# Performance work log

Hardware: AMD Instinct MI355X
Metric: run time of the kernel (lower is better)

The kernel has to match this reference:

```python
import jax, jax.numpy as jnp
import numpy as np

EPS = 1e-12  # torch F.normalize eps

def _l2norm(t):
    # normalize along last axis, clamp norm like torch.nn.functional.normalize
    n = jnp.sqrt(jnp.sum(t * t, axis=-1, keepdims=True))
    return t / jnp.maximum(n, EPS)

def setup_inputs() -> dict:
    key = jax.random.key(0)
    k1, k2, k3 = jax.random.split(key, 3)
    B, N, C, h = 4, 16384, 512, 8
    x = jax.random.normal(k1, (B, N, C), dtype=jnp.float32)
    qkv_w = jax.random.normal(k2, (C, 3 * C), dtype=jnp.float32) * 0.02
    proj_w = jax.random.normal(k3, (C, C), dtype=jnp.float32) * 0.02
    proj_b = jnp.zeros((C,), dtype=jnp.float32)
    temperature = jnp.ones((h, 1, 1), dtype=jnp.float32)  # temperature_init=1.0
    return {"x": x, "H": 128, "W": 128, "qkv_w": qkv_w,
            "proj_w": proj_w, "proj_b": proj_b, "temperature": temperature}

def reference(x, H, W, qkv_w, proj_w, proj_b, temperature):
    B, N, C = x.shape
    h = temperature.shape[0]
    d = C // h
    qkv = (x @ qkv_w).reshape(B, N, 3, h, d)          # [B,N,3,h,d]
    qkv = jnp.transpose(qkv, (2, 0, 3, 1, 4))         # [3,B,h,N,d]
    q, k, v = qkv[0], qkv[1], qkv[2]
    # channel attention: transpose to [B,h,d,N], normalize over tokens
    q = _l2norm(jnp.swapaxes(q, -2, -1))              # [B,h,d,N]
    k = _l2norm(jnp.swapaxes(k, -2, -1))              # [B,h,d,N]
    v = jnp.swapaxes(v, -2, -1)                       # [B,h,d,N]
    attn = jnp.einsum('bhdn,bhen->bhde', q, k) * temperature  # [B,h,d,d]
    attn = jax.nn.softmax(attn, axis=-1)
    out = jnp.einsum('bhde,bhen->bhdn', attn, v)      # [B,h,d,N]
    out = jnp.transpose(out, (0, 3, 1, 2)).reshape(B, N, C)
    return out @ proj_w + proj_b
```

## Files before the change

kernel.cpp:

```cpp
#include <hip/hip_runtime.h>
#include <stdint.h>
#include <stddef.h>


typedef unsigned short u16;
typedef __attribute__((ext_vector_type(8))) unsigned short u16x8;
typedef __attribute__((ext_vector_type(8))) __bf16 bf16x8;
typedef __attribute__((ext_vector_type(4))) float f32x4;

#define B_DIM 4
#define N_TOK 16384
#define C_DIM 512
#define CQ3   1536
#define NROWS 65536

__device__ __forceinline__ u16 f2bf(float f) {
  union { float f; uint32_t u; } v; v.f = f;
  uint32_t r = v.u + 0x7FFFu + ((v.u >> 16) & 1u);
  return (u16)(r >> 16);
}
__device__ __forceinline__ float bf2f(u16 u) {
  union { uint32_t u; float f; } v; v.u = ((uint32_t)u) << 16;
  return v.f;
}
__device__ __forceinline__ bf16x8 as_bf16x8(u16x8 u) {
  union { u16x8 u; bf16x8 b; } v; v.u = u; return v.b;
}
__device__ __forceinline__ bf16x8 ldfrag(const u16* p) {
  return as_bf16x8(*(const u16x8*)p);
}
__device__ __forceinline__ void gl_lds16(const void* g, void* l) {
  __builtin_amdgcn_global_load_lds(
      (const __attribute__((address_space(1))) uint32_t*)g,
      (__attribute__((address_space(3))) uint32_t*)l, 16, 0, 0);
}

__global__ __launch_bounds__(256) void k_wswz(const float* __restrict__ w, u16* __restrict__ wl) {
  int g = blockIdx.x * 256 + threadIdx.x;
  int c8 = g / CQ3, j = g - c8 * CQ3;
  u16x8 o;
#pragma unroll
  for (int i = 0; i < 8; ++i) o[i] = f2bf(w[(size_t)(c8 * 8 + i) * CQ3 + j]);
  *(u16x8*)(wl + (size_t)g * 8) = o;
}
__global__ __launch_bounds__(256) void k_pswz(const float* __restrict__ w, u16* __restrict__ pwl) {
  int g = blockIdx.x * 256 + threadIdx.x;
  int d8 = g >> 9, j = g & 511;
  u16x8 o;
#pragma unroll
  for (int i = 0; i < 8; ++i) o[i] = f2bf(w[(size_t)(d8 * 8 + i) * 512 + j]);
  *(u16x8*)(pwl + (size_t)g * 8) = o;
}
__global__ __launch_bounds__(256) void k_vswz(const float* __restrict__ w, u16* __restrict__ vA) {
  int g = blockIdx.x * 256 + threadIdx.x;
  int c = g >> 6, q = g & 63;
  const float* s = w + (size_t)c * CQ3 + 1024 + q * 8;
  float4 v0 = *(const float4*)s, v1 = *(const float4*)(s + 4);
  u16x8 o;
  o[0] = f2bf(v0.x); o[1] = f2bf(v0.y); o[2] = f2bf(v0.z); o[3] = f2bf(v0.w);
  o[4] = f2bf(v1.x); o[5] = f2bf(v1.y); o[6] = f2bf(v1.z); o[7] = f2bf(v1.w);
  *(u16x8*)(vA + (size_t)g * 8) = o;
}

__global__ __launch_bounds__(256) void k_xc(const float* __restrict__ x,
                                            u16* __restrict__ xb,
                                            u16* __restrict__ xbT) {
  __shared__ __align__(16) u16 T[16384];
  const int bi = blockIdx.x;
  const int b = bi >> 9, tt = (bi >> 2) & 127, ct = bi & 3;
  const int n0 = tt * 128, c0 = ct * 128;
  const int tid = threadIdx.x;
  const int cb8 = (tid & 15) * 8;
  const int tch = tid >> 4;
  const float* src = x + (size_t)(b * N_TOK + n0 + tch * 8) * C_DIM + c0 + cb8;
  float v[8][8];
#pragma unroll
  for (int j = 0; j < 8; ++j) {
    float4 a0 = *(const float4*)(src + (size_t)j * C_DIM);
    float4 a1 = *(const float4*)(src + (size_t)j * C_DIM + 4);
    v[j][0] = a0.x; v[j][1] = a0.y; v[j][2] = a0.z; v[j][3] = a0.w;
    v[j][4] = a1.x; v[j][5] = a1.y; v[j][6] = a1.z; v[j][7] = a1.w;
  }
  u16* xbd = xb + (size_t)(b * N_TOK + n0 + tch * 8) * C_DIM + c0 + cb8;
#pragma unroll
  for (int j = 0; j < 8; ++j) {
    u16x8 o;
#pragma unroll
    for (int i = 0; i < 8; ++i) o[i] = f2bf(v[j][i]);
    *(u16x8*)(xbd + (size_t)j * C_DIM) = o;
  }
#pragma unroll
  for (int i = 0; i < 8; ++i) {
    int c_loc = cb8 + i;
    int pc = tch ^ (tid & 15);
    u16x8 o;
#pragma unroll
    for (int j = 0; j < 8; ++j) o[j] = f2bf(v[j][i]);
    *(u16x8*)&T[c_loc * 128 + pc * 8] = o;
  }
  __syncthreads();
#pragma unroll
  for (int t = 0; t < 8; ++t) {
    int c_loc = t * 16 + (tid >> 4);
    int lch = tid & 15;
    int pc = lch ^ ((c_loc >> 3) & 15);
    u16x8 o = *(const u16x8*)&T[c_loc * 128 + pc * 8];
    *(u16x8*)&xbT[(size_t)(b * C_DIM + c0 + c_loc) * N_TOK + n0 + lch * 8] = o;
  }
}

__global__ __launch_bounds__(256, 4) void k_g(const u16* __restrict__ xbT, u16* __restrict__ Gp) {
  __shared__ __align__(16) u16 As[8192];
  __shared__ __align__(16) u16 Bs[8192];
  const int tid = threadIdx.x, lane = tid & 63, wid = tid >> 6;
  const int orig = blockIdx.x;
  const int wg = (orig & 7) * 128 + (orig >> 3);
  const int kc = wg >> 6, rem = wg & 63;
  const int b = rem >> 4, ti = (rem >> 2) & 3, tj = rem & 3;
  const u16* abase = xbT + ((size_t)b * 512 + ti * 128) * N_TOK + kc * 1024;
  const u16* bbase = xbT + ((size_t)b * 512 + tj * 128) * N_TOK + kc * 1024;
  const int wr = wid >> 1, wc = wid & 1;

  f32x4 acc[4][4];
#pragma unroll
  for (int i = 0; i < 4; ++i)
#pragma unroll
    for (int j = 0; j < 4; ++j) acc[i][j] = (f32x4){0.f, 0.f, 0.f, 0.f};

  for (int kb = 0; kb < 16; ++kb) {
#pragma unroll
    for (int s4 = 0; s4 < 4; ++s4) {
      int slot = s4 * 256 + tid;
      int idx = slot >> 3, kblk = slot & 7;
      int kcol = kb * 64 + ((kblk ^ (idx & 7)) * 8);
      gl_lds16(abase + (size_t)idx * N_TOK + kcol, &As[slot * 8]);
      gl_lds16(bbase + (size_t)idx * N_TOK + kcol, &Bs[slot * 8]);
    }
    __syncthreads();
#pragma unroll
    for (int kk = 0; kk < 2; ++kk) {
      const int krow = kk * 4 + (lane >> 4);
      const int pk = krow ^ (lane & 7);
      bf16x8 af[4], bfr[4];
#pragma unroll
      for (int t = 0; t < 4; ++t)
        af[t] = *(const bf16x8*)&As[((wr * 64 + t * 16 + (lane & 15)) * 8 + pk) * 8];
#pragma unroll
      for (int t = 0; t < 4; ++t)
        bfr[t] = *(const bf16x8*)&Bs[((wc * 64 + t * 16 + (lane & 15)) * 8 + pk) * 8];
#pragma unroll
      for (int mt = 0; mt < 4; ++mt)
#pragma unroll
        for (int nt = 0; nt < 4; ++nt)
          acc[mt][nt] = __builtin_amdgcn_mfma_f32_16x16x32_bf16(af[mt], bfr[nt], acc[mt][nt], 0, 0, 0);
    }
    __syncthreads();
  }
  u16* wsl = (wid < 2) ? &As[wid * 4096] : &Bs[(wid - 2) * 4096];
#pragma unroll
  for (int mt = 0; mt < 4; ++mt)
#pragma unroll
    for (int nt = 0; nt < 4; ++nt)
#pragma unroll
      for (int r = 0; r < 4; ++r) {
        int row = mt * 16 + (lane >> 4) * 4 + r;
        int col = nt * 16 + (lane & 15);
        int slot = (col >> 3) ^ (row & 7);
        wsl[row * 64 + slot * 8 + (col & 7)] = f2bf(acc[mt][nt][r]);
      }
  u16* gdst = Gp + (size_t)(kc * 4 + b) * 262144;
#pragma unroll
  for (int it = 0; it < 8; ++it) {
    int rr = it * 8 + (lane >> 3);
    int slot = (lane & 7) ^ (rr & 7);
    *(u16x8*)&gdst[(size_t)(ti * 128 + wr * 64 + rr) * 512 + tj * 128 + wc * 64 + (lane & 7) * 8] =
        *(const u16x8*)&wsl[rr * 64 + slot * 8];
  }
}

__global__ __launch_bounds__(256) void k_red(const u16* __restrict__ Gp, u16* __restrict__ G) {
  int g = blockIdx.x * 256 + threadIdx.x;
  int b = g >> 15;
  size_t off = (size_t)(g & 32767) * 8;
  float s[8];
#pragma unroll
  for (int i = 0; i < 8; ++i) s[i] = 0.f;
  for (int kc = 0; kc < 16; ++kc) {
    u16x8 v = *(const u16x8*)(Gp + (size_t)(kc * 4 + b) * 262144 + off);
#pragma unroll
    for (int i = 0; i < 8; ++i) s[i] += bf2f(v[i]);
  }
  u16x8 o;
#pragma unroll
  for (int i = 0; i < 8; ++i) o[i] = f2bf(s[i]);
  *(u16x8*)(G + (size_t)b * 262144 + off) = o;
}

__global__ __launch_bounds__(256) void k_gq(const u16* __restrict__ G,
                                            const u16* __restrict__ wl,
                                            u16* __restrict__ Gqk) {
  const int bi = blockIdx.x;
  const int b = bi >> 5, mt = (bi >> 3) & 3, nt2 = bi & 7;
  const int m0 = mt * 128, n0 = nt2 * 128;
  const int lane = threadIdx.x & 63, w = threadIdx.x >> 6;
  f32x4 acc[8][2];
#pragma unroll
  for (int i = 0; i < 8; ++i) { acc[i][0] = (f32x4){0,0,0,0}; acc[i][1] = (f32x4){0,0,0,0}; }
  for (int ks = 0; ks < 16; ++ks) {
    bf16x8 bfr[2];
#pragma unroll
    for (int nf = 0; nf < 2; ++nf)
      bfr[nf] = ldfrag(wl + ((size_t)(ks * 4 + (lane >> 4)) * CQ3 + n0 + w * 32 + nf * 16 + (lane & 15)) * 8);
#pragma unroll
    for (int mf = 0; mf < 8; ++mf) {
      bf16x8 af = ldfrag(G + (size_t)b * 262144 + (size_t)(m0 + mf * 16 + (lane & 15)) * 512 + ks * 32 + (lane >> 4) * 8);
#pragma unroll
      for (int nf = 0; nf < 2; ++nf)
        acc[mf][nf] = __builtin_amdgcn_mfma_f32_16x16x32_bf16(af, bfr[nf], acc[mf][nf], 0, 0, 0);
    }
  }
#pragma unroll
  for (int mf = 0; mf < 8; ++mf)
#pragma unroll
    for (int nf = 0; nf < 2; ++nf)
#pragma unroll
      for (int r = 0; r < 4; ++r) {
        int d = m0 + mf * 16 + (lane >> 4) * 4 + r;
        int j = n0 + w * 32 + nf * 16 + (lane & 15);
        Gqk[(size_t)b * 524288 + ((size_t)(d >> 3) * 1024 + j) * 8 + (d & 7)] = f2bf(acc[mf][nf][r]);
      }
}

__global__ __launch_bounds__(256) void k_s2(const u16* __restrict__ Gqk,
                                            const u16* __restrict__ wl,
                                            const u16* __restrict__ pwl,
                                            const float* __restrict__ temp,
                                            u16* __restrict__ Ml) {
  __shared__ float Ssh[4][4096];
  __shared__ u16 At[64 * 72];
  __shared__ float ssqsh[128];
  __shared__ float rqk[128];
  const int tid = threadIdx.x, lane = tid & 63, w = tid >> 6;
  const int bh = blockIdx.x, b = bh >> 3, hh = bh & 7;
  if (tid < 128) ssqsh[tid] = 0.f;

  f32x4 acc[4][4];
#pragma unroll
  for (int i = 0; i < 4; ++i)
#pragma unroll
    for (int j = 0; j < 4; ++j) acc[i][j] = (f32x4){0.f, 0.f, 0.f, 0.f};
  for (int ks = 0; ks < 4; ++ks) {
    const int crow = w * 16 + ks * 4 + (lane >> 4);
    bf16x8 aq[4], bk[4];
#pragma unroll
    for (int mf = 0; mf < 4; ++mf)
      aq[mf] = ldfrag(wl + ((size_t)crow * CQ3 + hh * 64 + mf * 16 + (lane & 15)) * 8);
#pragma unroll
    for (int nf = 0; nf < 4; ++nf)
      bk[nf] = ldfrag(Gqk + (size_t)b * 524288 + ((size_t)crow * 1024 + 512 + hh * 64 + nf * 16 + (lane & 15)) * 8);
#pragma unroll
    for (int mf = 0; mf < 4; ++mf)
#pragma unroll
      for (int nf = 0; nf < 4; ++nf)
        acc[mf][nf] = __builtin_amdgcn_mfma_f32_16x16x32_bf16(aq[mf], bk[nf], acc[mf][nf], 0, 0, 0);
  }
#pragma unroll
  for (int mf = 0; mf < 4; ++mf)
#pragma unroll
    for (int nf = 0; nf < 4; ++nf)
#pragma unroll
      for (int r = 0; r < 4; ++r)
        Ssh[w][(mf * 16 + (lane >> 4) * 4 + r) * 64 + nf * 16 + (lane & 15)] = acc[mf][nf][r];
  __syncthreads();
  for (int idx = tid; idx < 4096; idx += 256)
    Ssh[0][idx] = Ssh[0][idx] + Ssh[1][idx] + Ssh[2][idx] + Ssh[3][idx];

  {
    const int d = tid & 63, part = tid >> 6;
    float sq = 0.f, sk = 0.f;
    for (int co = 0; co < 16; ++co) {
      int c8 = part * 16 + co;
      u16x8 wq = *(const u16x8*)(wl + ((size_t)c8 * CQ3 + hh * 64 + d) * 8);
      u16x8 gq = *(const u16x8*)(Gqk + (size_t)b * 524288 + ((size_t)c8 * 1024 + hh * 64 + d) * 8);
      u16x8 wk = *(const u16x8*)(wl + ((size_t)c8 * CQ3 + 512 + hh * 64 + d) * 8);
      u16x8 gk = *(const u16x8*)(Gqk + (size_t)b * 524288 + ((size_t)c8 * 1024 + 512 + hh * 64 + d) * 8);
#pragma unroll
      for (int i = 0; i < 8; ++i) {
        sq += bf2f(wq[i]) * bf2f(gq[i]);
        sk += bf2f(wk[i]) * bf2f(gk[i]);
      }
    }
    atomicAdd(&ssqsh[d], sq);
    atomicAdd(&ssqsh[64 + d], sk);
  }
  __syncthreads();
  if (tid < 128) rqk[tid] = 1.f / fmaxf(sqrtf(fmaxf(ssqsh[tid], 0.f)), 1e-12f);
  __syncthreads();

  {
    const float tp = temp[hh];
    const int d = tid >> 2, q4 = tid & 3;
    float vals[16];
    float mx = -3.0e38f;
    const float rqd = rqk[d];
#pragma unroll
    for (int i = 0; i < 16; ++i) {
      float v = Ssh[0][d * 64 + q4 * 16 + i] * rqd * rqk[64 + q4 * 16 + i] * tp;
      vals[i] = v; mx = fmaxf(mx, v);
    }
    mx = fmaxf(mx, __shfl_xor(mx, 1));
    mx = fmaxf(mx, __shfl_xor(mx, 2));
    float sum = 0.f;
#pragma unroll
    for (int i = 0; i < 16; ++i) { vals[i] = __expf(vals[i] - mx); sum += vals[i]; }
    sum += __shfl_xor(sum, 1);
    sum += __shfl_xor(sum, 2);
    const float inv = 1.f / sum;
#pragma unroll
    for (int i = 0; i < 16; ++i) At[(q4 * 16 + i) * 72 + d] = f2bf(vals[i] * inv);
  }
  __syncthreads();

  f32x4 acc2[4][8];
#pragma unroll
  for (int i = 0; i < 4; ++i)
#pragma unroll
    for (int j = 0; j < 8; ++j) acc2[i][j] = (f32x4){0.f, 0.f, 0.f, 0.f};
#pragma unroll
  for (int s = 0; s < 2; ++s) {
    bf16x8 af[4], bfr[8];
#pragma unroll
    for (int mf = 0; mf < 4; ++mf)
      af[mf] = *(const bf16x8*)&At[(mf * 16 + (lane & 15)) * 72 + s * 32 + (lane >> 4) * 8];
#pragma unroll
    for (int nf = 0; nf < 8; ++nf)
      bfr[nf] = ldfrag(pwl + ((size_t)(hh * 8 + s * 4 + (lane >> 4)) * 512 + w * 128 + nf * 16 + (lane & 15)) * 8);
#pragma unroll
    for (int mf = 0; mf < 4; ++mf)
#pragma unroll
      for (int nf = 0; nf < 8; ++nf)
        acc2[mf][nf] = __builtin_amdgcn_mfma_f32_16x16x32_bf16(af[mf], bfr[nf], acc2[mf][nf], 0, 0, 0);
  }
#pragma unroll
  for (int mf = 0; mf < 4; ++mf)
#pragma unroll
    for (int nf = 0; nf < 8; ++nf)
#pragma unroll
      for (int r = 0; r < 4; ++r) {
        int e = mf * 16 + (lane >> 4) * 4 + r;
        int j = w * 128 + nf * 16 + (lane & 15);
        int cc = hh * 64 + e;
        Ml[(size_t)b * 262144 + ((size_t)(cc >> 3) * 512 + j) * 8 + (cc & 7)] = f2bf(acc2[mf][nf][r]);
      }
}

__global__ __launch_bounds__(256) void k_p(const u16* __restrict__ vA,
                                           const u16* __restrict__ Ml,
                                           u16* __restrict__ Pl) {
  const int bi = blockIdx.x;
  const int b = bi >> 4, ct = (bi >> 2) & 3, jt = bi & 3;
  const int m0 = ct * 128, j0 = jt * 128;
  const int lane = threadIdx.x & 63, w = threadIdx.x >> 6;
  f32x4 acc[8][2];
#pragma unroll
  for (int i = 0; i < 8; ++i) { acc[i][0] = (f32x4){0,0,0,0}; acc[i][1] = (f32x4){0,0,0,0}; }
  for (int ks = 0; ks < 16; ++ks) {
    bf16x8 bfr[2];
#pragma unroll
    for (int nf = 0; nf < 2; ++nf)
      bfr[nf] = ldfrag(Ml + (size_t)b * 262144 + ((size_t)(ks * 4 + (lane >> 4)) * 512 + j0 + w * 32 + nf * 16 + (lane & 15)) * 8);
#pragma unroll
    for (int mf = 0; mf < 8; ++mf) {
      bf16x8 af = ldfrag(vA + (size_t)(m0 + mf * 16 + (lane & 15)) * 512 + ks * 32 + (lane >> 4) * 8);
#pragma unroll
      for (int nf = 0; nf < 2; ++nf)
        acc[mf][nf] = __builtin_amdgcn_mfma_f32_16x16x32_bf16(af, bfr[nf], acc[mf][nf], 0, 0, 0);
    }
  }
#pragma unroll
  for (int mf = 0; mf < 8; ++mf)
#pragma unroll
    for (int nf = 0; nf < 2; ++nf)
#pragma unroll
      for (int r = 0; r < 4; ++r) {
        int c = m0 + mf * 16 + (lane >> 4) * 4 + r;
        int j = j0 + w * 32 + nf * 16 + (lane & 15);
        Pl[(size_t)b * 262144 + ((size_t)(c >> 3) * 512 + j) * 8 + (c & 7)] = f2bf(acc[mf][nf][r]);
      }
}

__global__ __launch_bounds__(256, 4) void k_out(const u16* __restrict__ xb,
                                                const u16* __restrict__ Pl,
                                                const float* __restrict__ pb,
                                                float* __restrict__ out) {
  __shared__ __align__(16) u16 As[8192];
  __shared__ __align__(16) u16 Bs[8192];
  const int tid = threadIdx.x;
  const int orig = blockIdx.x;
  const int wg = (orig & 7) * 256 + (orig >> 3);
  const int cb = wg & 3, rb = wg >> 2;
  const int row0 = rb * 128, col0 = cb * 128;
  const int b = rb >> 7;
  const int lane = tid & 63, wid = tid >> 6;
  const int wr = wid >> 1, wc = wid & 1;
  float bias[4];
#pragma unroll
  for (int nt = 0; nt < 4; ++nt) bias[nt] = pb[col0 + wc * 64 + nt * 16 + (lane & 15)];

  f32x4 acc[4][4];
#pragma unroll
  for (int i = 0; i < 4; ++i)
#pragma unroll
    for (int j = 0; j < 4; ++j) acc[i][j] = (f32x4){0.f, 0.f, 0.f, 0.f};

  const u16* pbase = Pl + (size_t)b * 262144;
  for (int kb = 0; kb < 8; ++kb) {
#pragma unroll
    for (int s4 = 0; s4 < 4; ++s4) {
      int slot = s4 * 256 + tid;
      int idx = slot >> 3, kblk = slot & 7;
      gl_lds16(xb + (size_t)(row0 + idx) * C_DIM + kb * 64 + ((kblk ^ (idx & 7)) * 8), &As[slot * 8]);
      int kblkB = slot >> 7, j = slot & 127;
      gl_lds16(pbase + ((size_t)(kb * 8 + kblkB) * 512 + col0 + j) * 8, &Bs[slot * 8]);
    }
    __syncthreads();
#pragma unroll
    for (int kk = 0; kk < 2; ++kk) {
      const int krow = kk * 4 + (lane >> 4);
      const int pk = krow ^ (lane & 7);
      bf16x8 af[4], bfr[4];
#pragma unroll
      for (int t = 0; t < 4; ++t)
        af[t] = *(const bf16x8*)&As[((wr * 64 + t * 16 + (lane & 15)) * 8 + pk) * 8];
#pragma unroll
      for (int t = 0; t < 4; ++t)
        bfr[t] = *(const bf16x8*)&Bs[(krow * 128 + wc * 64 + t * 16 + (lane & 15)) * 8];
#pragma unroll
      for (int mt = 0; mt < 4; ++mt)
#pragma unroll
        for (int nt = 0; nt < 4; ++nt)
          acc[mt][nt] = __builtin_amdgcn_mfma_f32_16x16x32_bf16(af[mt], bfr[nt], acc[mt][nt], 0, 0, 0);
    }
    __syncthreads();
  }
  float* slice = (wid < 2) ? (float*)&As[wid * 4096] : (float*)&Bs[(wid - 2) * 4096];
#pragma unroll
  for (int half = 0; half < 2; ++half) {
#pragma unroll
    for (int m2 = 0; m2 < 2; ++m2)
#pragma unroll
      for (int nt = 0; nt < 4; ++nt)
#pragma unroll
        for (int r = 0; r < 4; ++r) {
          int row = m2 * 16 + (lane >> 4) * 4 + r;
          int col = nt * 16 + (lane & 15);
          int slot = (col >> 2) ^ (row & 15);
          slice[row * 64 + slot * 4 + (col & 3)] = acc[half * 2 + m2][nt][r] + bias[nt];
        }
#pragma unroll
    for (int it = 0; it < 8; ++it) {
      int rr = it * 4 + (lane >> 4);
      int s = (lane & 15) ^ (rr & 15);
      *(float4*)&out[(size_t)(row0 + wr * 64 + half * 32 + rr) * C_DIM + col0 + wc * 64 + (lane & 15) * 4] =
          *(const float4*)&slice[rr * 64 + s * 4];
    }
  }
}

extern "C" void kernel_launch(void* const* d_in, const int* in_sizes, int n_in,
                              void* d_out, int out_size, void* d_ws, size_t ws_size,
                              hipStream_t stream) {
  const float* x      = (const float*)d_in[0];
  const float* qkv_w  = (const float*)d_in[3];
  const float* proj_w = (const float*)d_in[4];
  const float* proj_b = (const float*)d_in[5];
  const float* temp   = (const float*)d_in[6];
  float* out = (float*)d_out;

  char* ws = (char*)d_ws;
  u16* xb  = (u16*)(ws);
  u16* xbT = (u16*)(ws + 67108864);
  u16* wl  = (u16*)(ws + 134217728);
  u16* pwl = (u16*)(ws + 135790592);
  u16* vA  = (u16*)(ws + 136314880);
  u16* Gp  = (u16*)(ws + 136839168);
  u16* G   = (u16*)(ws + 170393600);
  u16* Gqk = (u16*)(ws + 172490752);
  u16* Ml  = (u16*)(ws + 176685056);
  u16* Pl  = (u16*)(ws + 178782208);

  k_wswz<<<384, 256, 0, stream>>>(qkv_w, wl);
  k_pswz<<<128, 256, 0, stream>>>(proj_w, pwl);
  k_vswz<<<128, 256, 0, stream>>>(qkv_w, vA);
  k_xc<<<2048, 256, 0, stream>>>(x, xb, xbT);
  k_g<<<1024, 256, 0, stream>>>(xbT, Gp);
  k_red<<<512, 256, 0, stream>>>(Gp, G);
  k_gq<<<128, 256, 0, stream>>>(G, wl, Gqk);
  k_s2<<<32, 256, 0, stream>>>(Gqk, wl, pwl, temp, Ml);
  k_p<<<64, 256, 0, stream>>>(vA, Ml, Pl);
  k_out<<<2048, 256, 0, stream>>>(xb, Pl, proj_b, out);
}
```

Baseline: 245.6 us.

## Double-buffer LDS staging in Gram and output GEMMs; merge weight-prep kernels

Adds ping-pong LDS buffers to k_g and k_out so the next K-tile's global-to-LDS loads are issued before the MFMA work on the current tile, with an explicit vmcnt drain before each barrier. This aims to hide global load latency behind compute. The three weight-swizzle kernels are merged into one launch to cut launch overhead. Doubling LDS to 64KB per block and dropping the occupancy hint of 4 may lower occupancy.

After: 250.4 us. About the same (+2.0%).

```diff
diff --git a/kernel.cpp b/kernel.cpp
--- a/kernel.cpp
+++ b/kernel.cpp
@@ -34,32 +34,37 @@
       (const __attribute__((address_space(1))) uint32_t*)g,
       (__attribute__((address_space(3))) uint32_t*)l, 16, 0, 0);
 }
-
-__global__ __launch_bounds__(256) void k_wswz(const float* __restrict__ w, u16* __restrict__ wl) {
+#define VMDRAIN asm volatile("s_waitcnt vmcnt(0)" ::: "memory")
+
+__global__ __launch_bounds__(256) void k_prep(const float* __restrict__ qkv_w,
+                                              const float* __restrict__ proj_w,
+                                              u16* __restrict__ wl,
+                                              u16* __restrict__ pwl,
+                                              u16* __restrict__ vA) {
   int g = blockIdx.x * 256 + threadIdx.x;
-  int c8 = g / CQ3, j = g - c8 * CQ3;
-  u16x8 o;
-#pragma unroll
-  for (int i = 0; i < 8; ++i) o[i] = f2bf(w[(size_t)(c8 * 8 + i) * CQ3 + j]);
-  *(u16x8*)(wl + (size_t)g * 8) = o;
-}
-__global__ __launch_bounds__(256) void k_pswz(const float* __restrict__ w, u16* __restrict__ pwl) {
-  int g = blockIdx.x * 256 + threadIdx.x;
-  int d8 = g >> 9, j = g & 511;
-  u16x8 o;
-#pragma unroll
-  for (int i = 0; i < 8; ++i) o[i] = f2bf(w[(size_t)(d8 * 8 + i) * 512 + j]);
-  *(u16x8*)(pwl + (size_t)g * 8) = o;
-}
-__global__ __launch_bounds__(256) void k_vswz(const float* __restrict__ w, u16* __restrict__ vA) {
-  int g = blockIdx.x * 256 + threadIdx.x;
-  int c = g >> 6, q = g & 63;
-  const float* s = w + (size_t)c * CQ3 + 1024 + q * 8;
-  float4 v0 = *(const float4*)s, v1 = *(const float4*)(s + 4);
-  u16x8 o;
-  o[0] = f2bf(v0.x); o[1] = f2bf(v0.y); o[2] = f2bf(v0.z); o[3] = f2bf(v0.w);
-  o[4] = f2bf(v1.x); o[5] = f2bf(v1.y); o[6] = f2bf(v1.z); o[7] = f2bf(v1.w);
-  *(u16x8*)(vA + (size_t)g * 8) = o;
+  if (g < 98304) {
+    int c8 = g / CQ3, j = g - c8 * CQ3;
+    u16x8 o;
+#pragma unroll
+    for (int i = 0; i < 8; ++i) o[i] = f2bf(qkv_w[(size_t)(c8 * 8 + i) * CQ3 + j]);
+    *(u16x8*)(wl + (size_t)g * 8) = o;
+  } else if (g < 131072) {
+    int gg = g - 98304;
+    int d8 = gg >> 9, j = gg & 511;
+    u16x8 o;
+#pragma unroll
+    for (int i = 0; i < 8; ++i) o[i] = f2bf(proj_w[(size_t)(d8 * 8 + i) * 512 + j]);
+    *(u16x8*)(pwl + (size_t)gg * 8) = o;
+  } else {
+    int gg = g - 131072;
+    int c = gg >> 6, q = gg & 63;
+    const float* s = qkv_w + (size_t)c * CQ3 + 1024 + q * 8;
+    float4 v0 = *(const float4*)s, v1 = *(const float4*)(s + 4);
+    u16x8 o;
+    o[0] = f2bf(v0.x); o[1] = f2bf(v0.y); o[2] = f2bf(v0.z); o[3] = f2bf(v0.w);
+    o[4] = f2bf(v1.x); o[5] = f2bf(v1.y); o[6] = f2bf(v1.z); o[7] = f2bf(v1.w);
+    *(u16x8*)(vA + (size_t)gg * 8) = o;
+  }
 }
 
 __global__ __launch_bounds__(256) void k_xc(const float* __restrict__ x,
@@ -109,9 +114,9 @@
   }
 }
 
-__global__ __launch_bounds__(256, 4) void k_g(const u16* __restrict__ xbT, u16* __restrict__ Gp) {
-  __shared__ __align__(16) u16 As[8192];
-  __shared__ __align__(16) u16 Bs[8192];
+__global__ __launch_bounds__(256) void k_g(const u16* __restrict__ xbT, u16* __restrict__ Gp) {
+  __shared__ __align__(16) u16 As[2][8192];
+  __shared__ __align__(16) u16 Bs[2][8192];
   const int tid = threadIdx.x, lane = tid & 63, wid = tid >> 6;
   const int orig = blockIdx.x;
   const int wg = (orig & 7) * 128 + (orig >> 3);
@@ -121,22 +126,31 @@
   const u16* bbase = xbT + ((size_t)b * 512 + tj * 128) * N_TOK + kc * 1024;
   const int wr = wid >> 1, wc = wid & 1;
 
-  f32x4 acc[4][4];
-#pragma unroll
-  for (int i = 0; i < 4; ++i)
-#pragma unroll
-    for (int j = 0; j < 4; ++j) acc[i][j] = (f32x4){0.f, 0.f, 0.f, 0.f};
-
-  for (int kb = 0; kb < 16; ++kb) {
+  const int sidx = tid >> 1, skblk0 = (tid & 1) * 4;
+
+  auto stage = [&](int kb, int buf) {
 #pragma unroll
     for (int s4 = 0; s4 < 4; ++s4) {
       int slot = s4 * 256 + tid;
       int idx = slot >> 3, kblk = slot & 7;
       int kcol = kb * 64 + ((kblk ^ (idx & 7)) * 8);
-      gl_lds16(abase + (size_t)idx * N_TOK + kcol, &As[slot * 8]);
-      gl_lds16(bbase + (size_t)idx * N_TOK + kcol, &Bs[slot * 8]);
-    }
-    __syncthreads();
+      gl_lds16(abase + (size_t)idx * N_TOK + kcol, &As[buf][slot * 8]);
+      gl_lds16(bbase + (size_t)idx * N_TOK + kcol, &Bs[buf][slot * 8]);
+    }
+  };
+
+  f32x4 acc[4][4];
+#pragma unroll
+  for (int i = 0; i < 4; ++i)
+#pragma unroll
+    for (int j = 0; j < 4; ++j) acc[i][j] = (f32x4){0.f, 0.f, 0.f, 0.f};
+
+  stage(0, 0);
+  VMDRAIN;
+  __syncthreads();
+  for (int kb = 0; kb < 16; ++kb) {
+    const int cur = kb & 1;
+    if (kb < 15) stage(kb + 1, cur ^ 1);
 #pragma unroll
     for (int kk = 0; kk < 2; ++kk) {
       const int krow = kk * 4 + (lane >> 4);
@@ -144,19 +158,20 @@
       bf16x8 af[4], bfr[4];
 #pragma unroll
       for (int t = 0; t < 4; ++t)
-        af[t] = *(const bf16x8*)&As[((wr * 64 + t * 16 + (lane & 15)) * 8 + pk) * 8];
+        af[t] = *(const bf16x8*)&As[cur][((wr * 64 + t * 16 + (lane & 15)) * 8 + pk) * 8];
 #pragma unroll
       for (int t = 0; t < 4; ++t)
-        bfr[t] = *(const bf16x8*)&Bs[((wc * 64 + t * 16 + (lane & 15)) * 8 + pk) * 8];
+        bfr[t] = *(const bf16x8*)&Bs[cur][((wc * 64 + t * 16 + (lane & 15)) * 8 + pk) * 8];
 #pragma unroll
       for (int mt = 0; mt < 4; ++mt)
 #pragma unroll
         for (int nt = 0; nt < 4; ++nt)
           acc[mt][nt] = __builtin_amdgcn_mfma_f32_16x16x32_bf16(af[mt], bfr[nt], acc[mt][nt], 0, 0, 0);
     }
+    if (kb < 15) VMDRAIN;
     __syncthreads();
   }
-  u16* wsl = (wid < 2) ? &As[wid * 4096] : &Bs[(wid - 2) * 4096];
+  u16* wsl = &As[0][0] + wid * 4096;
 #pragma unroll
   for (int mt = 0; mt < 4; ++mt)
 #pragma unroll
@@ -389,12 +404,12 @@
       }
 }
 
-__global__ __launch_bounds__(256, 4) void k_out(const u16* __restrict__ xb,
-                                                const u16* __restrict__ Pl,
-                                                const float* __restrict__ pb,
-                                                float* __restrict__ out) {
-  __shared__ __align__(16) u16 As[8192];
-  __shared__ __align__(16) u16 Bs[8192];
+__global__ __launch_bounds__(256) void k_out(const u16* __restrict__ xb,
+                                             const u16* __restrict__ Pl,
+                                             const float* __restrict__ pb,
+                                             float* __restrict__ out) {
+  __shared__ __align__(16) u16 As[2][8192];
+  __shared__ __align__(16) u16 Bs[2][8192];
   const int tid = threadIdx.x;
   const int orig = blockIdx.x;
   const int wg = (orig & 7) * 256 + (orig >> 3);
@@ -407,23 +422,31 @@
 #pragma unroll
   for (int nt = 0; nt < 4; ++nt) bias[nt] = pb[col0 + wc * 64 + nt * 16 + (lane & 15)];
 
-  f32x4 acc[4][4];
-#pragma unroll
-  for (int i = 0; i < 4; ++i)
-#pragma unroll
-    for (int j = 0; j < 4; ++j) acc[i][j] = (f32x4){0.f, 0.f, 0.f, 0.f};
-
   const u16* pbase = Pl + (size_t)b * 262144;
-  for (int kb = 0; kb < 8; ++kb) {
+  auto stage = [&](int kb, int buf) {
 #pragma unroll
     for (int s4 = 0; s4 < 4; ++s4) {
       int slot = s4 * 256 + tid;
       int idx = slot >> 3, kblk = slot & 7;
-      gl_lds16(xb + (size_t)(row0 + idx) * C_DIM + kb * 64 + ((kblk ^ (idx & 7)) * 8), &As[slot * 8]);
+      gl_lds16(xb + (size_t)(row0 + idx) * C_DIM + kb * 64 + ((kblk ^ (idx & 7)) * 8),
+               &As[buf][slot * 8]);
       int kblkB = slot >> 7, j = slot & 127;
-      gl_lds16(pbase + ((size_t)(kb * 8 + kblkB) * 512 + col0 + j) * 8, &Bs[slot * 8]);
-    }
-    __syncthreads();
+      gl_lds16(pbase + ((size_t)(kb * 8 + kblkB) * 512 + col0 + j) * 8, &Bs[buf][slot * 8]);
+    }
+  };
+
+  f32x4 acc[4][4];
+#pragma unroll
+  for (int i = 0; i < 4; ++i)
+#pragma unroll
+    for (int j = 0; j < 4; ++j) acc[i][j] = (f32x4){0.f, 0.f, 0.f, 0.f};
+
+  stage(0, 0);
+  VMDRAIN;
+  __syncthreads();
+  for (int kb = 0; kb < 8; ++kb) {
+    const int cur = kb & 1;
+    if (kb < 7) stage(kb + 1, cur ^ 1);
 #pragma unroll
     for (int kk = 0; kk < 2; ++kk) {
       const int krow = kk * 4 + (lane >> 4);
@@ -431,19 +454,20 @@
       bf16x8 af[4], bfr[4];
 #pragma unroll
       for (int t = 0; t < 4; ++t)
-        af[t] = *(const bf16x8*)&As[((wr * 64 + t * 16 + (lane & 15)) * 8 + pk) * 8];
+        af[t] = *(const bf16x8*)&As[cur][((wr * 64 + t * 16 + (lane & 15)) * 8 + pk) * 8];
 #pragma unroll
       for (int t = 0; t < 4; ++t)
-        bfr[t] = *(const bf16x8*)&Bs[(krow * 128 + wc * 64 + t * 16 + (lane & 15)) * 8];
+        bfr[t] = *(const bf16x8*)&Bs[cur][(krow * 128 + wc * 64 + t * 16 + (lane & 15)) * 8];
 #pragma unroll
       for (int mt = 0; mt < 4; ++mt)
 #pragma unroll
         for (int nt = 0; nt < 4; ++nt)
           acc[mt][nt] = __builtin_amdgcn_mfma_f32_16x16x32_bf16(af[mt], bfr[nt], acc[mt][nt], 0, 0, 0);
     }
+    if (kb < 7) VMDRAIN;
     __syncthreads();
   }
-  float* slice = (wid < 2) ? (float*)&As[wid * 4096] : (float*)&Bs[(wid - 2) * 4096];
+  float* slice = (float*)(&As[0][0]) + wid * 2048;
 #pragma unroll
   for (int half = 0; half < 2; ++half) {
 #pragma unroll
@@ -489,10 +513,8 @@
   u16* Ml  = (u16*)(ws + 176685056);
   u16* Pl  = (u16*)(ws + 178782208);
 
-  k_wswz<<<384, 256, 0, stream>>>(qkv_w, wl);
-  k_pswz<<<128, 256, 0, stream>>>(proj_w, pwl);
-  k_vswz<<<128, 256, 0, stream>>>(qkv_w, vA);
   k_xc<<<2048, 256, 0, stream>>>(x, xb, xbT);
+  k_prep<<<640, 256, 0, stream>>>(qkv_w, proj_w, wl, pwl, vA);
   k_g<<<1024, 256, 0, stream>>>(xbT, Gp);
   k_red<<<512, 256, 0, stream>>>(Gp, G);
   k_gq<<<128, 256, 0, stream>>>(G, wl, Gqk);
```
